# Kernel optimization log

Measured on AMD Instinct MI355X. Metric: run time of the kernel, lower is better.

Reference implementation:

```python
import jax, jax.numpy as jnp
import numpy as np

B, T, C = 4, 4096, 1024
E, K, H = 8, 2, 4 * 1024


def setup_inputs() -> dict:
    key = jax.random.key(0)
    ks = jax.random.split(key, 7)
    s = lambda *sh: 1.0 / np.sqrt(sh[-2] if len(sh) > 1 else sh[-1])
    x = jax.random.normal(ks[0], (B, T, C), dtype=jnp.float32)
    router_w = jax.random.normal(ks[1], (C, E), dtype=jnp.float32) * (1.0 / np.sqrt(C))
    router_b = jnp.zeros((E,), dtype=jnp.float32)
    w1 = jax.random.normal(ks[2], (E, C, H), dtype=jnp.float32) * (1.0 / np.sqrt(C))
    b1 = jnp.zeros((E, H), dtype=jnp.float32)
    w2 = jax.random.normal(ks[3], (E, H, C), dtype=jnp.float32) * (1.0 / np.sqrt(H))
    b2 = jnp.zeros((E, C), dtype=jnp.float32)
    return {"x": x, "router_w": router_w, "router_b": router_b,
            "w1": w1, "b1": b1, "w2": w2, "b2": b2}


def reference(x, router_w, router_b, w1, b1, w2, b2):
    Bq, Tq, Cq = x.shape
    N = Bq * Tq
    logits = jnp.einsum('btc,ce->bte', x, router_w) + router_b      # [B,T,E]
    probs = jax.nn.softmax(logits, axis=-1)
    topk_vals, topk_idx = jax.lax.top_k(probs, K)                   # [B,T,K]
    x_flat = x.reshape(N, Cq)
    idx_flat = topk_idx.reshape(N, K)
    vals_flat1d = topk_vals.reshape(-1)                             # [N*K]
    # Faithful to original: weight for token t is topk_vals.view(-1)[t]
    w_tok = vals_flat1d[jnp.arange(N)]                              # [N]
    output = jnp.zeros_like(x_flat)
    for e in range(E):
        mask = (idx_flat == e).any(axis=-1)                         # [N] bool
        h = jax.nn.relu(x_flat @ w1[e] + b1[e])                     # [N,H]
        out_e = h @ w2[e] + b2[e]                                   # [N,C]
        output = output + (jnp.where(mask, w_tok, 0.0))[:, None] * out_e
    importance = probs.mean(axis=(0, 1))                            # [E]
    counts = jnp.zeros((E,), dtype=jnp.float32).at[idx_flat.reshape(-1)].add(1.0)
    load = counts / (N * K)
    aux_loss = (importance * load).sum()
    return output.reshape(Bq, Tq, Cq), aux_loss
```

## Files before the change

kernel.cpp:

```cpp
#include <hip/hip_runtime.h>
#include <hip/hip_bf16.h>

#define N_TOK 16384
#define C_DIM 1024
#define H_DIM 4096
#define E_NUM 8
#define NK_TOT 32768

typedef unsigned short u16;
typedef unsigned int u32;
typedef float f4 __attribute__((ext_vector_type(4)));
typedef __bf16 bf8 __attribute__((ext_vector_type(8)));

union V16 { f4 f; bf8 b; };

__device__ __forceinline__ u16 f2bf(float x) {
  u32 u = __builtin_bit_cast(u32, x);
  u = (u + 0x7fffu + ((u >> 16) & 1u)) >> 16;
  return (u16)u;
}

__global__ __launch_bounds__(256) void cvt_x_k(const float* __restrict__ src, u16* __restrict__ dst) {
  const size_t g = (size_t)blockIdx.x * 256 + threadIdx.x;
  const f4 v = ((const f4*)src)[g];
  u32 lo = (u32)f2bf(v[0]) | ((u32)f2bf(v[1]) << 16);
  u32 hi = (u32)f2bf(v[2]) | ((u32)f2bf(v[3]) << 16);
  ((uint2*)dst)[g] = make_uint2(lo, hi);
}

__global__ __launch_bounds__(256) void transpose_cvt_k(const float* __restrict__ src, u16* __restrict__ dst,
                                                       int R, int S) {
  __shared__ float tile[64][65];
  const size_t eoff = (size_t)blockIdx.z * R * S;
  const int s0 = blockIdx.x * 64, r0 = blockIdx.y * 64;
  for (int p = threadIdx.x; p < 4096; p += 256) {
    int r = p >> 6, s = p & 63;
    tile[r][s] = src[eoff + (size_t)(r0 + r) * S + (s0 + s)];
  }
  __syncthreads();
  for (int p = threadIdx.x; p < 4096; p += 256) {
    int sN = p >> 6, rN = p & 63;
    dst[eoff + (size_t)(s0 + sN) * R + (r0 + rN)] = f2bf(tile[rN][sN]);
  }
}

__global__ __launch_bounds__(256) void router_k(const float* __restrict__ x, const float* __restrict__ rw,
                                                const float* __restrict__ rb, int* __restrict__ idx,
                                                float* __restrict__ vals, u32* __restrict__ cnt,
                                                float* __restrict__ imp) {
  __shared__ float s_imp[E_NUM];
  __shared__ u32 s_cnt[E_NUM];
  if (threadIdx.x < E_NUM) { s_imp[threadIdx.x] = 0.f; s_cnt[threadIdx.x] = 0u; }
  __syncthreads();
  const int wave = threadIdx.x >> 6, lane = threadIdx.x & 63;
  const int t = blockIdx.x * 4 + wave;
  const float* xr = x + (size_t)t * C_DIM;
  float a[E_NUM] = {0.f, 0.f, 0.f, 0.f, 0.f, 0.f, 0.f, 0.f};
  for (int c = lane; c < C_DIM; c += 64) {
    float xv = xr[c];
    const float* w = rw + c * E_NUM;
#pragma unroll
    for (int e = 0; e < E_NUM; ++e) a[e] = fmaf(xv, w[e], a[e]);
  }
#pragma unroll
  for (int e = 0; e < E_NUM; ++e) {
#pragma unroll
    for (int off = 32; off > 0; off >>= 1) a[e] += __shfl_xor(a[e], off, 64);
  }
  if (lane == 0) {
    float p[E_NUM]; float m = -1e30f, s = 0.f;
#pragma unroll
    for (int e = 0; e < E_NUM; ++e) { p[e] = a[e] + rb[e]; m = fmaxf(m, p[e]); }
#pragma unroll
    for (int e = 0; e < E_NUM; ++e) { p[e] = expf(p[e] - m); s += p[e]; }
    const float inv = 1.f / s;
#pragma unroll
    for (int e = 0; e < E_NUM; ++e) p[e] *= inv;
    int e0 = 0; float v0 = p[0];
#pragma unroll
    for (int e = 1; e < E_NUM; ++e) if (p[e] > v0) { v0 = p[e]; e0 = e; }
    int e1 = -1; float v1 = -1e30f;
#pragma unroll
    for (int e = 0; e < E_NUM; ++e) if (e != e0 && p[e] > v1) { v1 = p[e]; e1 = e; }
    idx[2 * t] = e0; idx[2 * t + 1] = e1;
    vals[2 * t] = v0; vals[2 * t + 1] = v1;
    atomicAdd(&s_cnt[e0], 1u); atomicAdd(&s_cnt[e1], 1u);
#pragma unroll
    for (int e = 0; e < E_NUM; ++e) atomicAdd(&s_imp[e], p[e]);
  }
  __syncthreads();
  if (threadIdx.x < E_NUM) {
    atomicAdd(&cnt[threadIdx.x], s_cnt[threadIdx.x]);
    atomicAdd(&imp[threadIdx.x], s_imp[threadIdx.x]);
  }
}

__global__ void offsets_k(const u32* __restrict__ cnt, int* __restrict__ off) {
  if (threadIdx.x == 0) {
    int s = 0;
    for (int e = 0; e < E_NUM; ++e) { off[e] = s; s += (int)cnt[e]; }
    off[E_NUM] = s;
  }
}

__global__ __launch_bounds__(256) void scatter_k(const int* __restrict__ idx, u32* __restrict__ cursor,
                                                 int* __restrict__ tl) {
  __shared__ u32 lcnt[E_NUM];
  __shared__ u32 base[E_NUM];
  if (threadIdx.x < E_NUM) lcnt[threadIdx.x] = 0u;
  __syncthreads();
  const int t = blockIdx.x * 256 + threadIdx.x;
  const int e0 = idx[2 * t], e1 = idx[2 * t + 1];
  const u32 p0 = atomicAdd(&lcnt[e0], 1u);
  const u32 p1 = atomicAdd(&lcnt[e1], 1u);
  __syncthreads();
  if (threadIdx.x < E_NUM) base[threadIdx.x] = atomicAdd(&cursor[threadIdx.x], lcnt[threadIdx.x]);
  __syncthreads();
  tl[e0 * N_TOK + (int)(base[e0] + p0)] = t;
  tl[e1 * N_TOK + (int)(base[e1] + p1)] = t;
}

template <int MODE>
__global__ __launch_bounds__(256, 2) void moe_gemm(
    const u16* __restrict__ A_base, const u16* __restrict__ Bt, const float* __restrict__ bias,
    u16* __restrict__ h_out, float* out_acc, const int* __restrict__ token_list,
    const u32* __restrict__ counts, const int* __restrict__ offsets,
    int K_len, int B_stride, int B_ncap, int n_base, int k_off, int A_stride, int h_stride) {
  const int e = blockIdx.z;
  const int n_e = (int)counts[e];
  const int m0 = blockIdx.x * 128;
  if (m0 >= n_e) return;
  const int off_e = offsets[e];
  const int nb = blockIdx.y * 128;

  __shared__ u16 lA[4][128][8];
  __shared__ u16 lB[4][128][8];

  const int tid = threadIdx.x;
  const u16* a_src[2]; const u16* b_src[2];
  u16* a_dst[2]; u16* b_dst[2];
#pragma unroll
  for (int q = 0; q < 2; ++q) {
    int p = tid + q * 256;
    int kb = p & 3, r = p >> 2;
    int ar = m0 + r; if (ar > n_e - 1) ar = n_e - 1;
    size_t arow;
    if (MODE == 0) arow = (size_t)token_list[e * N_TOK + ar] * A_stride;
    else           arow = (size_t)(off_e + ar) * A_stride;
    a_src[q] = A_base + arow + kb * 8;
    b_src[q] = Bt + ((size_t)e * B_ncap + (n_base + nb + r)) * B_stride + k_off + kb * 8;
    a_dst[q] = &lA[kb][r][0];
    b_dst[q] = &lB[kb][r][0];
  }

  f4 acc[4][4];
#pragma unroll
  for (int i = 0; i < 4; ++i)
#pragma unroll
    for (int j = 0; j < 4; ++j) acc[i][j] = (f4){0.f, 0.f, 0.f, 0.f};

  const int lane = tid & 63;
  const int wave = tid >> 6;
  const int wm = (wave >> 1) * 64;
  const int wn = (wave & 1) * 64;
  const int quad = lane >> 4, l16 = lane & 15;

  const int iters = K_len >> 5;
  for (int it = 0; it < iters; ++it) {
    f4 va0 = *(const f4*)a_src[0];
    f4 va1 = *(const f4*)a_src[1];
    f4 vb0 = *(const f4*)b_src[0];
    f4 vb1 = *(const f4*)b_src[1];
    a_src[0] += 32; a_src[1] += 32; b_src[0] += 32; b_src[1] += 32;
    __syncthreads();
    *(f4*)a_dst[0] = va0; *(f4*)a_dst[1] = va1;
    *(f4*)b_dst[0] = vb0; *(f4*)b_dst[1] = vb1;
    __syncthreads();
    V16 af[4], bfr[4];
#pragma unroll
    for (int i = 0; i < 4; ++i) af[i].f = *(const f4*)&lA[quad][wm + i * 16 + l16][0];
#pragma unroll
    for (int j = 0; j < 4; ++j) bfr[j].f = *(const f4*)&lB[quad][wn + j * 16 + l16][0];
#pragma unroll
    for (int i = 0; i < 4; ++i)
#pragma unroll
      for (int j = 0; j < 4; ++j)
        acc[i][j] = __builtin_amdgcn_mfma_f32_16x16x32_bf16(af[i].b, bfr[j].b, acc[i][j], 0, 0, 0);
  }

#pragma unroll
  for (int i = 0; i < 4; ++i) {
    const int lm = wm + i * 16 + quad * 4;
#pragma unroll
    for (int j = 0; j < 4; ++j) {
      const int ncol = nb + wn + j * 16 + l16;
#pragma unroll
      for (int r = 0; r < 4; ++r) {
        const int row = m0 + lm + r;
        if (row < n_e) {
          float v = acc[i][j][r];
          if (MODE == 0) {
            v += bias[e * H_DIM + n_base + ncol];
            v = fmaxf(v, 0.f);
            h_out[(size_t)(off_e + row) * h_stride + ncol] = f2bf(v);
          } else {
            const int tok = token_list[e * N_TOK + row];
            atomicAdd(&out_acc[(size_t)tok * C_DIM + ncol], v);
          }
        }
      }
    }
  }
}

__global__ __launch_bounds__(256) void final_k(float* out, const float* __restrict__ vals,
                                               const int* __restrict__ idx, const float* __restrict__ b2,
                                               const u32* __restrict__ cnt, const float* __restrict__ imp) {
  const size_t g = (size_t)blockIdx.x * 256 + threadIdx.x;
  const int t = (int)(g >> 8);
  const int c4 = (int)(g & 255);
  const float w = vals[t];
  const int e0 = idx[2 * t], e1 = idx[2 * t + 1];
  f4 a = ((const f4*)out)[g];
  f4 u = ((const f4*)(b2 + (size_t)e0 * C_DIM))[c4];
  f4 v = ((const f4*)(b2 + (size_t)e1 * C_DIM))[c4];
  f4 r;
#pragma unroll
  for (int q = 0; q < 4; ++q) r[q] = w * (a[q] + u[q] + v[q]);
  ((f4*)out)[g] = r;
  if (g == 0) {
    float aux = 0.f;
    for (int e = 0; e < E_NUM; ++e)
      aux += (imp[e] / (float)N_TOK) * ((float)cnt[e] / (float)(N_TOK * 2));
    out[(size_t)N_TOK * C_DIM] = aux;
  }
}

extern "C" void kernel_launch(void* const* d_in, const int* in_sizes, int n_in,
                              void* d_out, int out_size, void* d_ws, size_t ws_size,
                              hipStream_t stream) {
  const float* x  = (const float*)d_in[0];
  const float* rw = (const float*)d_in[1];
  const float* rb = (const float*)d_in[2];
  const float* w1 = (const float*)d_in[3];
  const float* b1 = (const float*)d_in[4];
  const float* w2 = (const float*)d_in[5];
  const float* b2 = (const float*)d_in[6];
  float* out = (float*)d_out;

  char* ws = (char*)d_ws;
  size_t off = 0;
  auto alloc = [&](size_t bytes) -> void* {
    void* p = ws + off; off += (bytes + 255) & ~(size_t)255; return p;
  };
  u16* x_bf    = (u16*)alloc((size_t)N_TOK * C_DIM * 2);
  u16* w1t     = (u16*)alloc((size_t)E_NUM * H_DIM * C_DIM * 2);
  u16* w2t     = (u16*)alloc((size_t)E_NUM * C_DIM * H_DIM * 2);
  int* tl      = (int*)alloc((size_t)E_NUM * N_TOK * 4);
  int* idx     = (int*)alloc((size_t)N_TOK * 2 * 4);
  float* vals  = (float*)alloc((size_t)N_TOK * 2 * 4);
  u32* small   = (u32*)alloc(256);
  u32* cnt     = small;
  u32* cursor  = small + 8;
  float* imp   = (float*)(small + 16);
  int* offs    = (int*)(small + 24);

  size_t rem = (ws_size > off) ? ws_size - off : 0;
  int NC = 1;
  while (NC < 32 && (size_t)NK_TOT * (H_DIM / NC) * 2 > rem) NC <<= 1;
  const int Hc = H_DIM / NC;
  u16* h_buf = (u16*)(ws + off);

  hipMemsetAsync(out, 0, (size_t)out_size * sizeof(float), stream);
  hipMemsetAsync(small, 0, 256, stream);

  cvt_x_k<<<(N_TOK * C_DIM / 4) / 256, 256, 0, stream>>>(x, x_bf);
  transpose_cvt_k<<<dim3(H_DIM / 64, C_DIM / 64, E_NUM), 256, 0, stream>>>(w1, w1t, C_DIM, H_DIM);
  transpose_cvt_k<<<dim3(C_DIM / 64, H_DIM / 64, E_NUM), 256, 0, stream>>>(w2, w2t, H_DIM, C_DIM);
  router_k<<<N_TOK / 4, 256, 0, stream>>>(x, rw, rb, idx, vals, cnt, imp);
  offsets_k<<<1, 64, 0, stream>>>(cnt, offs);
  scatter_k<<<N_TOK / 256, 256, 0, stream>>>(idx, cursor, tl);

  for (int ci = 0; ci < NC; ++ci) {
    moe_gemm<0><<<dim3(128, Hc / 128, E_NUM), 256, 0, stream>>>(
        x_bf, w1t, b1, h_buf, nullptr, tl, cnt, offs,
         C_DIM,  C_DIM,  H_DIM,
         ci * Hc,  0,  C_DIM,  Hc);
    moe_gemm<1><<<dim3(128, C_DIM / 128, E_NUM), 256, 0, stream>>>(
        h_buf, w2t, nullptr, nullptr, out, tl, cnt, offs,
         Hc,  H_DIM,  C_DIM,
         0,  ci * Hc,  Hc,  0);
  }

  final_k<<<(N_TOK * C_DIM / 4) / 256, 256, 0, stream>>>(out, vals, idx, b2, cnt, imp);
}
```

Before: 1.618 ms.

## Load GEMM tiles directly to LDS with XOR swizzle and K-step 64

Replaces the register-staged global-to-LDS copy with direct global_load_lds transfers, so tile data no longer passes through VGPRs. The LDS layout becomes a row-major 128x64 tile with an XOR swizzle on 16-byte slots to avoid bank conflicts. The K step doubles from 32 to 64, halving the number of barriers per tile. Loads are still not double-buffered, so global latency stays exposed between the two barriers.

Result: faster. 1.306 ms (-19.3%).

```diff
diff --git a/kernel.cpp b/kernel.cpp
--- a/kernel.cpp
+++ b/kernel.cpp
@@ -133,24 +133,27 @@
   const int off_e = offsets[e];
   const int nb = blockIdx.y * 128;
 
-  __shared__ u16 lA[4][128][8];
-  __shared__ u16 lB[4][128][8];
+  __shared__ u16 lA[128 * 64];
+  __shared__ u16 lB[128 * 64];
 
   const int tid = threadIdx.x;
-  const u16* a_src[2]; const u16* b_src[2];
-  u16* a_dst[2]; u16* b_dst[2];
-#pragma unroll
-  for (int q = 0; q < 2; ++q) {
-    int p = tid + q * 256;
-    int kb = p & 3, r = p >> 2;
+  const int lane = tid & 63;
+  const int wave = tid >> 6;
+
+  const int sub = lane >> 3;
+  const int c16 = lane & 7;
+  const int gslot = c16 ^ sub;
+  const u16* a_src[4];
+  const u16* b_src[4];
+#pragma unroll
+  for (int q = 0; q < 4; ++q) {
+    const int r = q * 32 + wave * 8 + sub;
     int ar = m0 + r; if (ar > n_e - 1) ar = n_e - 1;
     size_t arow;
     if (MODE == 0) arow = (size_t)token_list[e * N_TOK + ar] * A_stride;
     else           arow = (size_t)(off_e + ar) * A_stride;
-    a_src[q] = A_base + arow + kb * 8;
-    b_src[q] = Bt + ((size_t)e * B_ncap + (n_base + nb + r)) * B_stride + k_off + kb * 8;
-    a_dst[q] = &lA[kb][r][0];
-    b_dst[q] = &lB[kb][r][0];
+    a_src[q] = A_base + arow + gslot * 8;
+    b_src[q] = Bt + ((size_t)e * B_ncap + (n_base + nb + r)) * B_stride + k_off + gslot * 8;
   }
 
   f4 acc[4][4];
@@ -159,33 +162,43 @@
 #pragma unroll
     for (int j = 0; j < 4; ++j) acc[i][j] = (f4){0.f, 0.f, 0.f, 0.f};
 
-  const int lane = tid & 63;
-  const int wave = tid >> 6;
+  const int quad = lane >> 4, l16 = lane & 15;
   const int wm = (wave >> 1) * 64;
   const int wn = (wave & 1) * 64;
-  const int quad = lane >> 4, l16 = lane & 15;
-
-  const int iters = K_len >> 5;
+  const int p7 = l16 & 7;
+
+  const int iters = K_len >> 6;
   for (int it = 0; it < iters; ++it) {
-    f4 va0 = *(const f4*)a_src[0];
-    f4 va1 = *(const f4*)a_src[1];
-    f4 vb0 = *(const f4*)b_src[0];
-    f4 vb1 = *(const f4*)b_src[1];
-    a_src[0] += 32; a_src[1] += 32; b_src[0] += 32; b_src[1] += 32;
+#pragma unroll
+    for (int q = 0; q < 4; ++q) {
+      __builtin_amdgcn_global_load_lds(
+          (const __attribute__((address_space(1))) void*)a_src[q],
+          (__attribute__((address_space(3))) void*)(&lA[q * 2048 + wave * 512]),
+          16, 0, 0);
+      __builtin_amdgcn_global_load_lds(
+          (const __attribute__((address_space(1))) void*)b_src[q],
+          (__attribute__((address_space(3))) void*)(&lB[q * 2048 + wave * 512]),
+          16, 0, 0);
+      a_src[q] += 64; b_src[q] += 64;
+    }
     __syncthreads();
-    *(f4*)a_dst[0] = va0; *(f4*)a_dst[1] = va1;
-    *(f4*)b_dst[0] = vb0; *(f4*)b_dst[1] = vb1;
+
+#pragma unroll
+    for (int kk = 0; kk < 2; ++kk) {
+      const int sl = (((kk << 2) | quad) ^ p7) * 8;
+      V16 af[4], bfr[4];
+#pragma unroll
+      for (int i = 0; i < 4; ++i) {
+        af[i].f  = *(const f4*)&lA[(wm + i * 16 + l16) * 64 + sl];
+        bfr[i].f = *(const f4*)&lB[(wn + i * 16 + l16) * 64 + sl];
+      }
+#pragma unroll
+      for (int i = 0; i < 4; ++i)
+#pragma unroll
+        for (int j = 0; j < 4; ++j)
+          acc[i][j] = __builtin_amdgcn_mfma_f32_16x16x32_bf16(af[i].b, bfr[j].b, acc[i][j], 0, 0, 0);
+    }
     __syncthreads();
-    V16 af[4], bfr[4];
-#pragma unroll
-    for (int i = 0; i < 4; ++i) af[i].f = *(const f4*)&lA[quad][wm + i * 16 + l16][0];
-#pragma unroll
-    for (int j = 0; j < 4; ++j) bfr[j].f = *(const f4*)&lB[quad][wn + j * 16 + l16][0];
-#pragma unroll
-    for (int i = 0; i < 4; ++i)
-#pragma unroll
-      for (int j = 0; j < 4; ++j)
-        acc[i][j] = __builtin_amdgcn_mfma_f32_16x16x32_bf16(af[i].b, bfr[j].b, acc[i][j], 0, 0, 0);
   }
 
 #pragma unroll
```

## Rewrite MoE GEMM with 256x256 tiles, direct-to-LDS loads and double buffering

Applied to the files above, without the earlier changes.

The grouped GEMM now uses 512-thread blocks with 256x256 output tiles and a K step of 64. Global-to-LDS copies go through global_load_lds and are double-buffered, interleaved with four MFMA phases under explicit vmcnt/barrier control. LDS rows are XOR-swizzled to avoid bank conflicts, and s_setprio is raised around MFMA bursts. This targets the old kernel's small tiles, lack of overlap and register-staged copies, but costs more registers and LDS, coarser tiles that waste work on partial expert tails, and delicate hand-written synchronization.

Result: slower. 1.858 ms (+14.9%).

```diff
diff --git a/kernel.cpp b/kernel.cpp
--- a/kernel.cpp
+++ b/kernel.cpp
@@ -13,6 +13,12 @@
 typedef __bf16 bf8 __attribute__((ext_vector_type(8)));
 
 union V16 { f4 f; bf8 b; };
+
+#define AS1 __attribute__((address_space(1)))
+#define AS3 __attribute__((address_space(3)))
+#define BARRIER() asm volatile("s_barrier" ::: "memory")
+#define LGKM0()   asm volatile("s_waitcnt lgkmcnt(0)" ::: "memory")
+#define VMC(n)    asm volatile("s_waitcnt vmcnt(" #n ")" ::: "memory")
 
 __device__ __forceinline__ u16 f2bf(float x) {
   u32 u = __builtin_bit_cast(u32, x);
@@ -121,96 +127,176 @@
 }
 
 template <int MODE>
-__global__ __launch_bounds__(256, 2) void moe_gemm(
+__global__ __launch_bounds__(512, 2) void moe_gemm(
     const u16* __restrict__ A_base, const u16* __restrict__ Bt, const float* __restrict__ bias,
     u16* __restrict__ h_out, float* out_acc, const int* __restrict__ token_list,
     const u32* __restrict__ counts, const int* __restrict__ offsets,
     int K_len, int B_stride, int B_ncap, int n_base, int k_off, int A_stride, int h_stride) {
   const int e = blockIdx.z;
   const int n_e = (int)counts[e];
-  const int m0 = blockIdx.x * 128;
+  const int m0 = blockIdx.x * 256;
   if (m0 >= n_e) return;
   const int off_e = offsets[e];
-  const int nb = blockIdx.y * 128;
-
-  __shared__ u16 lA[4][128][8];
-  __shared__ u16 lB[4][128][8];
+  const int nb = blockIdx.y * 256;
+
+  __shared__ u16 lds[2][4][8192];
 
   const int tid = threadIdx.x;
-  const u16* a_src[2]; const u16* b_src[2];
-  u16* a_dst[2]; u16* b_dst[2];
-#pragma unroll
-  for (int q = 0; q < 2; ++q) {
-    int p = tid + q * 256;
-    int kb = p & 3, r = p >> 2;
-    int ar = m0 + r; if (ar > n_e - 1) ar = n_e - 1;
-    size_t arow;
-    if (MODE == 0) arow = (size_t)token_list[e * N_TOK + ar] * A_stride;
-    else           arow = (size_t)(off_e + ar) * A_stride;
-    a_src[q] = A_base + arow + kb * 8;
-    b_src[q] = Bt + ((size_t)e * B_ncap + (n_base + nb + r)) * B_stride + k_off + kb * 8;
-    a_dst[q] = &lA[kb][r][0];
-    b_dst[q] = &lB[kb][r][0];
-  }
-
-  f4 acc[4][4];
-#pragma unroll
-  for (int i = 0; i < 4; ++i)
-#pragma unroll
-    for (int j = 0; j < 4; ++j) acc[i][j] = (f4){0.f, 0.f, 0.f, 0.f};
-
   const int lane = tid & 63;
   const int wave = tid >> 6;
-  const int wm = (wave >> 1) * 64;
-  const int wn = (wave & 1) * 64;
   const int quad = lane >> 4, l16 = lane & 15;
 
-  const int iters = K_len >> 5;
-  for (int it = 0; it < iters; ++it) {
-    f4 va0 = *(const f4*)a_src[0];
-    f4 va1 = *(const f4*)a_src[1];
-    f4 vb0 = *(const f4*)b_src[0];
-    f4 vb1 = *(const f4*)b_src[1];
-    a_src[0] += 32; a_src[1] += 32; b_src[0] += 32; b_src[1] += 32;
-    __syncthreads();
-    *(f4*)a_dst[0] = va0; *(f4*)a_dst[1] = va1;
-    *(f4*)b_dst[0] = vb0; *(f4*)b_dst[1] = vb1;
-    __syncthreads();
-    V16 af[4], bfr[4];
-#pragma unroll
-    for (int i = 0; i < 4; ++i) af[i].f = *(const f4*)&lA[quad][wm + i * 16 + l16][0];
-#pragma unroll
-    for (int j = 0; j < 4; ++j) bfr[j].f = *(const f4*)&lB[quad][wn + j * 16 + l16][0];
-#pragma unroll
-    for (int i = 0; i < 4; ++i)
-#pragma unroll
-      for (int j = 0; j < 4; ++j)
-        acc[i][j] = __builtin_amdgcn_mfma_f32_16x16x32_bf16(af[i].b, bfr[j].b, acc[i][j], 0, 0, 0);
-  }
-
-#pragma unroll
-  for (int i = 0; i < 4; ++i) {
-    const int lm = wm + i * 16 + quad * 4;
-#pragma unroll
-    for (int j = 0; j < 4; ++j) {
-      const int ncol = nb + wn + j * 16 + l16;
-#pragma unroll
-      for (int r = 0; r < 4; ++r) {
-        const int row = m0 + lm + r;
-        if (row < n_e) {
-          float v = acc[i][j][r];
-          if (MODE == 0) {
-            v += bias[e * H_DIM + n_base + ncol];
-            v = fmaxf(v, 0.f);
-            h_out[(size_t)(off_e + row) * h_stride + ncol] = f2bf(v);
-          } else {
-            const int tok = token_list[e * N_TOK + row];
-            atomicAdd(&out_acc[(size_t)tok * C_DIM + ncol], v);
+  u32 aoff[2][2], boff[2][2];
+#pragma unroll
+  for (int h = 0; h < 2; ++h)
+#pragma unroll
+    for (int q = 0; q < 2; ++q) {
+      const int p = q * 512 + tid;
+      const int lrow = p >> 3;
+      const int slot = (p & 7) ^ (lrow & 7);
+      int ar = m0 + h * 128 + lrow; if (ar > n_e - 1) ar = n_e - 1;
+      u32 arow;
+      if (MODE == 0) arow = (u32)token_list[e * N_TOK + ar] * (u32)A_stride;
+      else           arow = (u32)(off_e + ar) * (u32)A_stride;
+      aoff[h][q] = arow + slot * 8;
+      boff[h][q] = (u32)(e * B_ncap + (n_base + nb + h * 128 + lrow)) * (u32)B_stride
+                   + (u32)k_off + slot * 8;
+    }
+
+#define STAGE_A(BUF, HF, KB)                                                             \
+  {                                                                                      \
+    _Pragma("unroll") for (int q = 0; q < 2; ++q)                                        \
+      __builtin_amdgcn_global_load_lds(                                                  \
+          (const AS1 void*)(A_base + (size_t)aoff[HF][q] + (KB)),                        \
+          (AS3 void*)(&lds[BUF][(HF)*2][q * 4096 + wave * 512]), 16, 0, 0);              \
+  }
+#define STAGE_B(BUF, HF, KB)                                                             \
+  {                                                                                      \
+    _Pragma("unroll") for (int q = 0; q < 2; ++q)                                        \
+      __builtin_amdgcn_global_load_lds(                                                  \
+          (const AS1 void*)(Bt + (size_t)boff[HF][q] + (KB)),                            \
+          (AS3 void*)(&lds[BUF][(HF)*2 + 1][q * 4096 + wave * 512]), 16, 0, 0);          \
+  }
+
+  V16 af[4][2], bv0[2][2], bv1[2][2];
+  const int rA0 = (wave >> 2) * 64 + l16;
+  const int rB0 = (wave & 3) * 32 + l16;
+  const int p7 = l16 & 7;
+
+#define LD_A(BUF, HF)                                                                    \
+  {                                                                                      \
+    _Pragma("unroll") for (int i = 0; i < 4; ++i)                                        \
+      _Pragma("unroll") for (int kk = 0; kk < 2; ++kk)                                   \
+        af[i][kk].f = *(const f4*)&lds[BUF][(HF)*2]                                      \
+            [(rA0 + i * 16) * 64 + ((((kk << 2) | quad) ^ p7) * 8)];                     \
+  }
+#define LD_B(BUF, HF, BV)                                                                \
+  {                                                                                      \
+    _Pragma("unroll") for (int j = 0; j < 2; ++j)                                        \
+      _Pragma("unroll") for (int kk = 0; kk < 2; ++kk)                                   \
+        BV[j][kk].f = *(const f4*)&lds[BUF][(HF)*2 + 1]                                  \
+            [(rB0 + j * 16) * 64 + ((((kk << 2) | quad) ^ p7) * 8)];                     \
+  }
+
+  f4 acc[2][2][4][2];
+#pragma unroll
+  for (int qm = 0; qm < 2; ++qm)
+#pragma unroll
+    for (int qn = 0; qn < 2; ++qn)
+#pragma unroll
+      for (int i = 0; i < 4; ++i)
+#pragma unroll
+        for (int j = 0; j < 2; ++j) acc[qm][qn][i][j] = (f4){0.f, 0.f, 0.f, 0.f};
+
+#define MF(QM, QN, BV)                                                                   \
+  {                                                                                      \
+    __builtin_amdgcn_s_setprio(1);                                                       \
+    _Pragma("unroll") for (int i = 0; i < 4; ++i)                                        \
+      _Pragma("unroll") for (int j = 0; j < 2; ++j) {                                    \
+        acc[QM][QN][i][j] = __builtin_amdgcn_mfma_f32_16x16x32_bf16(                     \
+            af[i][0].b, BV[j][0].b, acc[QM][QN][i][j], 0, 0, 0);                         \
+        acc[QM][QN][i][j] = __builtin_amdgcn_mfma_f32_16x16x32_bf16(                     \
+            af[i][1].b, BV[j][1].b, acc[QM][QN][i][j], 0, 0, 0);                         \
+      }                                                                                  \
+    __builtin_amdgcn_s_setprio(0);                                                       \
+  }
+
+  const int T = K_len >> 6;
+
+  STAGE_A(0, 0, 0); STAGE_B(0, 0, 0); STAGE_A(0, 1, 0); STAGE_B(0, 1, 0);
+  STAGE_A(1, 0, 64); STAGE_B(1, 0, 64); STAGE_A(1, 1, 64);
+  VMC(6);
+  BARRIER();
+
+  for (int t = 0; t < T - 1; ++t) {
+    const int buf = t & 1;
+    const bool st2 = (t + 2 < T);
+    const int kb1 = (t + 1) * 64, kb2 = (t + 2) * 64;
+
+    LD_A(buf, 0); LD_B(buf, 0, bv0);
+    STAGE_B(buf ^ 1, 1, kb1);
+    BARRIER(); LGKM0();
+    MF(0, 0, bv0);
+    BARRIER();
+    LD_B(buf, 1, bv1);
+    if (st2) STAGE_A(buf, 0, kb2);
+    BARRIER(); LGKM0();
+    MF(0, 1, bv1);
+    BARRIER();
+    LD_A(buf, 1);
+    if (st2) STAGE_B(buf, 0, kb2);
+    BARRIER(); LGKM0();
+    MF(1, 0, bv0);
+    BARRIER();
+    if (st2) STAGE_A(buf, 1, kb2);
+    BARRIER(); LGKM0();
+    MF(1, 1, bv1);
+    if (st2) { VMC(6); } else { VMC(0); }
+    BARRIER();
+  }
+
+  {
+    const int buf = (T - 1) & 1;
+    LD_A(buf, 0); LD_B(buf, 0, bv0); LD_B(buf, 1, bv1);
+    MF(0, 0, bv0);
+    MF(0, 1, bv1);
+    LD_A(buf, 1);
+    MF(1, 0, bv0);
+    MF(1, 1, bv1);
+  }
+
+#pragma unroll
+  for (int qm = 0; qm < 2; ++qm)
+#pragma unroll
+    for (int i = 0; i < 4; ++i) {
+      const int lm = qm * 128 + (wave >> 2) * 64 + i * 16 + quad * 4;
+#pragma unroll
+      for (int qn = 0; qn < 2; ++qn)
+#pragma unroll
+        for (int j = 0; j < 2; ++j) {
+          const int ncol = nb + qn * 128 + (wave & 3) * 32 + j * 16 + l16;
+#pragma unroll
+          for (int r = 0; r < 4; ++r) {
+            const int row = m0 + lm + r;
+            if (row < n_e) {
+              float v = acc[qm][qn][i][j][r];
+              if (MODE == 0) {
+                v += bias[e * H_DIM + n_base + ncol];
+                v = fmaxf(v, 0.f);
+                h_out[(size_t)(off_e + row) * h_stride + ncol] = f2bf(v);
+              } else {
+                const int tok = token_list[e * N_TOK + row];
+                atomicAdd(&out_acc[(size_t)tok * C_DIM + ncol], v);
+              }
+            }
           }
         }
-      }
     }
-  }
+#undef STAGE_A
+#undef STAGE_B
+#undef LD_A
+#undef LD_B
+#undef MF
 }
 
 __global__ __launch_bounds__(256) void final_k(float* out, const float* __restrict__ vals,
@@ -267,7 +353,7 @@
 
   size_t rem = (ws_size > off) ? ws_size - off : 0;
   int NC = 1;
-  while (NC < 32 && (size_t)NK_TOT * (H_DIM / NC) * 2 > rem) NC <<= 1;
+  while (NC < 16 && (size_t)NK_TOT * (H_DIM / NC) * 2 > rem) NC <<= 1;
   const int Hc = H_DIM / NC;
   u16* h_buf = (u16*)(ws + off);
 
@@ -282,11 +368,11 @@
   scatter_k<<<N_TOK / 256, 256, 0, stream>>>(idx, cursor, tl);
 
   for (int ci = 0; ci < NC; ++ci) {
-    moe_gemm<0><<<dim3(128, Hc / 128, E_NUM), 256, 0, stream>>>(
+    moe_gemm<0><<<dim3(N_TOK / 256, Hc / 256, E_NUM), 512, 0, stream>>>(
         x_bf, w1t, b1, h_buf, nullptr, tl, cnt, offs,
          C_DIM,  C_DIM,  H_DIM,
          ci * Hc,  0,  C_DIM,  Hc);
-    moe_gemm<1><<<dim3(128, C_DIM / 128, E_NUM), 256, 0, stream>>>(
+    moe_gemm<1><<<dim3(N_TOK / 256, C_DIM / 256, E_NUM), 512, 0, stream>>>(
         h_buf, w2t, nullptr, nullptr, out, tl, cnt, offs,
          Hc,  H_DIM,  C_DIM,
          0,  ci * Hc,  Hc,  0);
```

## Triple-buffer GEMM with direct global-to-LDS loads and fold epilogue into init

Applied to the files above, without the earlier changes.

The MoE GEMM mainloop now uses global_load_lds to copy tiles straight into LDS, triple-buffered with a prefetch distance of two, and a single barrier per k-step gated by vmcnt. This replaces the register round-trip and the two barriers per iteration. The LDS layout changes to row-major 32-wide k slices, and launch bounds rise to 3 blocks/CU. The output memset and final scaling kernel are replaced by an init kernel that writes the weighted biases, and the second GEMM scales by the token weight before its atomic add. This removes a full read-modify-write pass over the output, at the cost of an extra multiply per atomic and more LDS and register pressure.

Result: no change. 1.594 ms (-1.5%).

```diff
diff --git a/kernel.cpp b/kernel.cpp
--- a/kernel.cpp
+++ b/kernel.cpp
@@ -13,6 +13,9 @@
 typedef __bf16 bf8 __attribute__((ext_vector_type(8)));
 
 union V16 { f4 f; bf8 b; };
+
+#define AS1 __attribute__((address_space(1)))
+#define AS3 __attribute__((address_space(3)))
 
 __device__ __forceinline__ u16 f2bf(float x) {
   u32 u = __builtin_bit_cast(u32, x);
@@ -120,11 +123,34 @@
   tl[e1 * N_TOK + (int)(base[e1] + p1)] = t;
 }
 
+__global__ __launch_bounds__(256) void init_out_k(float* out, const float* __restrict__ vals,
+                                                  const int* __restrict__ idx, const float* __restrict__ b2,
+                                                  const u32* __restrict__ cnt, const float* __restrict__ imp) {
+  const size_t g = (size_t)blockIdx.x * 256 + threadIdx.x;
+  const int t = (int)(g >> 8);
+  const int c4 = (int)(g & 255);
+  const float w = vals[t];
+  const int e0 = idx[2 * t], e1 = idx[2 * t + 1];
+  f4 u = ((const f4*)(b2 + (size_t)e0 * C_DIM))[c4];
+  f4 v = ((const f4*)(b2 + (size_t)e1 * C_DIM))[c4];
+  f4 r;
+#pragma unroll
+  for (int q = 0; q < 4; ++q) r[q] = w * (u[q] + v[q]);
+  ((f4*)out)[g] = r;
+  if (g == 0) {
+    float aux = 0.f;
+    for (int e = 0; e < E_NUM; ++e)
+      aux += (imp[e] / (float)N_TOK) * ((float)cnt[e] / (float)(N_TOK * 2));
+    out[(size_t)N_TOK * C_DIM] = aux;
+  }
+}
+
 template <int MODE>
-__global__ __launch_bounds__(256, 2) void moe_gemm(
+__global__ __launch_bounds__(256, 3) void moe_gemm(
     const u16* __restrict__ A_base, const u16* __restrict__ Bt, const float* __restrict__ bias,
     u16* __restrict__ h_out, float* out_acc, const int* __restrict__ token_list,
     const u32* __restrict__ counts, const int* __restrict__ offsets,
+    const float* __restrict__ wtok,
     int K_len, int B_stride, int B_ncap, int n_base, int k_off, int A_stride, int h_stride) {
   const int e = blockIdx.z;
   const int n_e = (int)counts[e];
@@ -133,25 +159,39 @@
   const int off_e = offsets[e];
   const int nb = blockIdx.y * 128;
 
-  __shared__ u16 lA[4][128][8];
-  __shared__ u16 lB[4][128][8];
+  __shared__ u16 lA[3][128 * 32];
+  __shared__ u16 lB[3][128 * 32];
 
   const int tid = threadIdx.x;
-  const u16* a_src[2]; const u16* b_src[2];
-  u16* a_dst[2]; u16* b_dst[2];
+  const int lane = tid & 63;
+  const int wave = tid >> 6;
+
+  const u16* a_src[2];
+  const u16* b_src[2];
 #pragma unroll
   for (int q = 0; q < 2; ++q) {
-    int p = tid + q * 256;
-    int kb = p & 3, r = p >> 2;
+    const int p = q * 256 + tid;
+    const int r = p >> 2;
+    const int sl = p & 3;
     int ar = m0 + r; if (ar > n_e - 1) ar = n_e - 1;
     size_t arow;
     if (MODE == 0) arow = (size_t)token_list[e * N_TOK + ar] * A_stride;
     else           arow = (size_t)(off_e + ar) * A_stride;
-    a_src[q] = A_base + arow + kb * 8;
-    b_src[q] = Bt + ((size_t)e * B_ncap + (n_base + nb + r)) * B_stride + k_off + kb * 8;
-    a_dst[q] = &lA[kb][r][0];
-    b_dst[q] = &lB[kb][r][0];
-  }
+    a_src[q] = A_base + arow + sl * 8;
+    b_src[q] = Bt + ((size_t)e * B_ncap + (n_base + nb + r)) * B_stride + k_off + sl * 8;
+  }
+
+  auto STAGE = [&](int buf, int kb) {
+#pragma unroll
+    for (int q = 0; q < 2; ++q) {
+      __builtin_amdgcn_global_load_lds(
+          (const AS1 void*)(a_src[q] + kb),
+          (AS3 void*)(&lA[buf][q * 2048 + wave * 512]), 16, 0, 0);
+      __builtin_amdgcn_global_load_lds(
+          (const AS1 void*)(b_src[q] + kb),
+          (AS3 void*)(&lB[buf][q * 2048 + wave * 512]), 16, 0, 0);
+    }
+  };
 
   f4 acc[4][4];
 #pragma unroll
@@ -159,33 +199,37 @@
 #pragma unroll
     for (int j = 0; j < 4; ++j) acc[i][j] = (f4){0.f, 0.f, 0.f, 0.f};
 
-  const int lane = tid & 63;
-  const int wave = tid >> 6;
+  const int quad = lane >> 4, l16 = lane & 15;
   const int wm = (wave >> 1) * 64;
   const int wn = (wave & 1) * 64;
-  const int quad = lane >> 4, l16 = lane & 15;
-
-  const int iters = K_len >> 5;
-  for (int it = 0; it < iters; ++it) {
-    f4 va0 = *(const f4*)a_src[0];
-    f4 va1 = *(const f4*)a_src[1];
-    f4 vb0 = *(const f4*)b_src[0];
-    f4 vb1 = *(const f4*)b_src[1];
-    a_src[0] += 32; a_src[1] += 32; b_src[0] += 32; b_src[1] += 32;
-    __syncthreads();
-    *(f4*)a_dst[0] = va0; *(f4*)a_dst[1] = va1;
-    *(f4*)b_dst[0] = vb0; *(f4*)b_dst[1] = vb1;
-    __syncthreads();
+  const int sl8 = quad * 8;
+
+  const int T = K_len >> 5;
+
+  STAGE(0, 0);
+  STAGE(1, 32);
+
+  int cb = 0, sb = 2;
+  for (int t = 0; t < T; ++t) {
+    if (t + 1 < T) { asm volatile("s_waitcnt vmcnt(4)" ::: "memory"); }
+    else           { asm volatile("s_waitcnt vmcnt(0)" ::: "memory"); }
+    asm volatile("s_barrier" ::: "memory");
+    if (t + 2 < T) {
+      STAGE(sb, (t + 2) * 32);
+      sb = (sb == 2) ? 0 : sb + 1;
+    }
     V16 af[4], bfr[4];
 #pragma unroll
-    for (int i = 0; i < 4; ++i) af[i].f = *(const f4*)&lA[quad][wm + i * 16 + l16][0];
-#pragma unroll
-    for (int j = 0; j < 4; ++j) bfr[j].f = *(const f4*)&lB[quad][wn + j * 16 + l16][0];
+    for (int i = 0; i < 4; ++i) {
+      af[i].f  = *(const f4*)&lA[cb][(wm + i * 16 + l16) * 32 + sl8];
+      bfr[i].f = *(const f4*)&lB[cb][(wn + i * 16 + l16) * 32 + sl8];
+    }
 #pragma unroll
     for (int i = 0; i < 4; ++i)
 #pragma unroll
       for (int j = 0; j < 4; ++j)
         acc[i][j] = __builtin_amdgcn_mfma_f32_16x16x32_bf16(af[i].b, bfr[j].b, acc[i][j], 0, 0, 0);
+    cb = (cb == 2) ? 0 : cb + 1;
   }
 
 #pragma unroll
@@ -205,34 +249,11 @@
             h_out[(size_t)(off_e + row) * h_stride + ncol] = f2bf(v);
           } else {
             const int tok = token_list[e * N_TOK + row];
-            atomicAdd(&out_acc[(size_t)tok * C_DIM + ncol], v);
+            atomicAdd(&out_acc[(size_t)tok * C_DIM + ncol], wtok[tok] * v);
           }
         }
       }
     }
-  }
-}
-
-__global__ __launch_bounds__(256) void final_k(float* out, const float* __restrict__ vals,
-                                               const int* __restrict__ idx, const float* __restrict__ b2,
-                                               const u32* __restrict__ cnt, const float* __restrict__ imp) {
-  const size_t g = (size_t)blockIdx.x * 256 + threadIdx.x;
-  const int t = (int)(g >> 8);
-  const int c4 = (int)(g & 255);
-  const float w = vals[t];
-  const int e0 = idx[2 * t], e1 = idx[2 * t + 1];
-  f4 a = ((const f4*)out)[g];
-  f4 u = ((const f4*)(b2 + (size_t)e0 * C_DIM))[c4];
-  f4 v = ((const f4*)(b2 + (size_t)e1 * C_DIM))[c4];
-  f4 r;
-#pragma unroll
-  for (int q = 0; q < 4; ++q) r[q] = w * (a[q] + u[q] + v[q]);
-  ((f4*)out)[g] = r;
-  if (g == 0) {
-    float aux = 0.f;
-    for (int e = 0; e < E_NUM; ++e)
-      aux += (imp[e] / (float)N_TOK) * ((float)cnt[e] / (float)(N_TOK * 2));
-    out[(size_t)N_TOK * C_DIM] = aux;
   }
 }
 
@@ -271,7 +292,6 @@
   const int Hc = H_DIM / NC;
   u16* h_buf = (u16*)(ws + off);
 
-  hipMemsetAsync(out, 0, (size_t)out_size * sizeof(float), stream);
   hipMemsetAsync(small, 0, 256, stream);
 
   cvt_x_k<<<(N_TOK * C_DIM / 4) / 256, 256, 0, stream>>>(x, x_bf);
@@ -280,17 +300,16 @@
   router_k<<<N_TOK / 4, 256, 0, stream>>>(x, rw, rb, idx, vals, cnt, imp);
   offsets_k<<<1, 64, 0, stream>>>(cnt, offs);
   scatter_k<<<N_TOK / 256, 256, 0, stream>>>(idx, cursor, tl);
+  init_out_k<<<(N_TOK * C_DIM / 4) / 256, 256, 0, stream>>>(out, vals, idx, b2, cnt, imp);
 
   for (int ci = 0; ci < NC; ++ci) {
     moe_gemm<0><<<dim3(128, Hc / 128, E_NUM), 256, 0, stream>>>(
-        x_bf, w1t, b1, h_buf, nullptr, tl, cnt, offs,
+        x_bf, w1t, b1, h_buf, nullptr, tl, cnt, offs, vals,
          C_DIM,  C_DIM,  H_DIM,
          ci * Hc,  0,  C_DIM,  Hc);
     moe_gemm<1><<<dim3(128, C_DIM / 128, E_NUM), 256, 0, stream>>>(
-        h_buf, w2t, nullptr, nullptr, out, tl, cnt, offs,
+        h_buf, w2t, nullptr, nullptr, out, tl, cnt, offs, vals,
          Hc,  H_DIM,  C_DIM,
          0,  ci * Hc,  Hc,  0);
   }
-
-  final_k<<<(N_TOK * C_DIM / 4) / 256, 256, 0, stream>>>(out, vals, idx, b2, cnt, imp);
-}
+}
```
